# Kernel optimization log

Measured on AMD Instinct MI355X. Metric: run time of the kernel, lower is better.

The kernel has to match this reference:

```python
import jax, jax.numpy as jnp
import numpy as np

B, C, H, W = 8, 64, 128, 128
OUT, K, PAD = 128, 9, 1  # 3x3 kernel -> K=9 taps


def setup_inputs() -> dict:
    key = jax.random.key(0)
    ks = jax.random.split(key, 6)
    x = jax.random.normal(ks[0], (B, C, H, W), dtype=jnp.float32)
    # trained-like params: small random offsets (std ~1-2 px) and mask logits
    w_offset = jax.random.normal(ks[1], (2 * K, C, 3, 3), dtype=jnp.float32) * 0.05
    b_offset = jax.random.normal(ks[2], (2 * K,), dtype=jnp.float32) * 0.1
    w_mask = jax.random.normal(ks[3], (K, C, 3, 3), dtype=jnp.float32) * 0.05
    b_mask = jax.random.normal(ks[4], (K,), dtype=jnp.float32) * 0.1
    w_conv = jax.random.normal(ks[5], (OUT, C, 3, 3), dtype=jnp.float32) * (1.0 / np.sqrt(C * 9))
    return {"x": x, "w_offset": w_offset, "b_offset": b_offset,
            "w_mask": w_mask, "b_mask": b_mask, "w_conv": w_conv}


def _conv3x3(x, w, b):
    out = jax.lax.conv_general_dilated(
        x, w, window_strides=(1, 1), padding=((PAD, PAD), (PAD, PAD)),
        dimension_numbers=("NCHW", "OIHW", "NCHW"))
    return out + b[None, :, None, None]


def _bilinear_gather(img, gy, gx):
    # img: [C,H,W]; gy,gx: [K,H,W] float sampling coords (zero outside bounds)
    C_, H_, W_ = img.shape
    y0 = jnp.floor(gy)
    x0 = jnp.floor(gx)
    wy = gy - y0
    wx = gx - x0
    img_flat = img.reshape(C_, H_ * W_)

    def corner(yi, xi, wgt):
        valid = ((yi >= 0) & (yi < H_) & (xi >= 0) & (xi < W_)).astype(img.dtype)
        yc = jnp.clip(yi, 0, H_ - 1).astype(jnp.int32)
        xc = jnp.clip(xi, 0, W_ - 1).astype(jnp.int32)
        v = img_flat[:, yc * W_ + xc]  # [C,K,H,W]
        return v * (wgt * valid)[None]

    return (corner(y0, x0, (1 - wy) * (1 - wx))
            + corner(y0, x0 + 1, (1 - wy) * wx)
            + corner(y0 + 1, x0, wy * (1 - wx))
            + corner(y0 + 1, x0 + 1, wy * wx))  # [C,K,H,W]


def reference(x, w_offset, b_offset, w_mask, b_mask, w_conv):
    offset = _conv3x3(x, w_offset, b_offset)                  # [B,18,H,W]
    mask = jax.nn.sigmoid(_conv3x3(x, w_mask, b_mask))        # [B,9,H,W]
    B_, C_, H_, W_ = x.shape
    # torchvision layout: channel 2k = dy, 2k+1 = dx for kernel tap k
    off = offset.reshape(B_, K, 2, H_, W_)
    dy, dx = off[:, :, 0], off[:, :, 1]                       # [B,K,H,W]
    ky, kx = jnp.meshgrid(jnp.arange(3, dtype=x.dtype),
                          jnp.arange(3, dtype=x.dtype), indexing="ij")
    gy = jnp.arange(H_, dtype=x.dtype)[None, None, :, None] - PAD + ky.reshape(1, K, 1, 1) + dy
    gx = jnp.arange(W_, dtype=x.dtype)[None, None, None, :] - PAD + kx.reshape(1, K, 1, 1) + dx
    sampled = jax.vmap(_bilinear_gather)(x, gy, gx)           # [B,C,K,H,W]
    sampled = sampled * mask[:, None]                         # modulated (DCNv2)
    out = jnp.einsum("bckhw,ock->bohw", sampled, w_conv.reshape(OUT, C_, K))
    return out
```

## Files before the change

kernel.cpp:

```cpp
#include <hip/hip_runtime.h>
#include <math.h>

#define Himg 128
#define Wimg 128
#define HW   16384
#define Cin  64
#define Kk   9
#define OUTC 128
#define Bsz  8

typedef __attribute__((ext_vector_type(8))) _Float16 half8;
typedef __attribute__((ext_vector_type(4))) float   floatx4;

#define SPL8(v) ((half8){(v),(v),(v),(v),(v),(v),(v),(v)})

__global__ __launch_bounds__(256) void prep(const float* __restrict__ x,
                                            const float* __restrict__ w_conv,
                                            const float* __restrict__ w_offset,
                                            const float* __restrict__ w_mask,
                                            _Float16* __restrict__ xt,
                                            _Float16* __restrict__ wpk_h,
                                            _Float16* __restrict__ wpk2) {
    __shared__ _Float16 tile[Cin][130];
    int t   = threadIdx.x;
    int bid = blockIdx.x;

    if (bid < 1024) {
        int b = bid >> 7;
        int h = bid & 127;
        const float* xb = x + (size_t)b * Cin * HW + (size_t)h * Wimg;
#pragma unroll
        for (int j = 0; j < 32; ++j) {
            int e = t + j * 256;
            int c = e >> 7;
            int w = e & 127;
            tile[c][w] = (_Float16)xb[(size_t)c * HW + w];
        }
        __syncthreads();
        unsigned* dst = (unsigned*)xt + ((size_t)b * HW + (size_t)h * Wimg) * 32;
#pragma unroll
        for (int j = 0; j < 16; ++j) {
            int d  = t + j * 256;
            int w  = d >> 5;
            int cp = d & 31;
            union { unsigned u; _Float16 hh[2]; } pk;
            pk.hh[0] = tile[2 * cp][w];
            pk.hh[1] = tile[2 * cp + 1][w];
            dst[d] = pk.u;
        }
        return;
    }

    if (bid < 1024 + 288) {
        int idx = (bid - 1024) * 256 + t;
        if (idx < Kk * Cin * OUTC) {
            int i    = idx & 7;
            int l    = (idx >> 3) & 63;
            int g    = idx >> 9;
            int mt   = g & 7;
            int ch   = g >> 3;
            int kq   = l >> 4;
            int ln16 = l & 15;
            int o    = mt * 16 + ln16;
            int kl   = kq * 8 + i;
            int c    = (ch & 1) * 32 + kl;
            int kt   = ch >> 1;
            wpk_h[idx] = (_Float16)w_conv[(o * Cin + c) * 9 + kt];
        }
        return;
    }

    {
        int idx = (bid - 1312) * 256 + t;
        if (idx < 18 * 32 * 32) {
            int i    = idx & 7;
            int l    = (idx >> 3) & 63;
            int g    = idx >> 9;
            int mt0  = g & 1;
            int ch   = g >> 1;
            int kq   = l >> 4;
            int ln16 = l & 15;
            int m    = mt0 * 16 + ln16;
            int kl   = kq * 8 + i;
            int c    = (ch & 1) * 32 + kl;
            int kt   = ch >> 1;
            float v = 0.0f;
            if (m < 18)      v = w_offset[(m * Cin + c) * 9 + kt];
            else if (m < 27) v = w_mask[((m - 18) * Cin + c) * 9 + kt];
            wpk2[idx] = (_Float16)v;
        }
    }
}

__global__ __launch_bounds__(256, 3) void deform_fused(
        const _Float16* __restrict__ xt, const _Float16* __restrict__ wpk_h,
        const _Float16* __restrict__ wpk2,
        const float* __restrict__ b_offset, const float* __restrict__ b_mask,
        float* __restrict__ out) {
    __shared__ _Float16 Vw[4][2][16][40];
    __shared__ float    Pw[4][32][16];

    int t    = threadIdx.x;
    int bid  = blockIdx.x;
    int b    = bid & 7;
    int pb   = bid >> 3;
    int pix0 = pb * 64;
    int h    = pix0 >> 7;
    int w0   = pix0 & 127;

    int lane = t & 63;
    int wv   = t >> 6;
    int q    = t >> 2;
    int qloc = (lane >> 2) & 15;
    int c4   = t & 3;
    int kq   = lane >> 4;
    int ln16 = lane & 15;

    const _Float16* xtb  = xt + (size_t)b * HW * Cin;
    const half8* wsrc    = (const half8*)wpk_h;
    const half8* w2src   = (const half8*)wpk2;

    floatx4 acc2_0 = (floatx4){0.f, 0.f, 0.f, 0.f};
    floatx4 acc2_1 = (floatx4){0.f, 0.f, 0.f, 0.f};

    half8 pvA, pvB;

#define LOADX0(chn, DST) { \
    const int ktn = (chn) >> 1, cgn = (chn) & 1; \
    int row = h + (ktn / 3) - 1; \
    int col = w0 + q + (ktn % 3) - 1; \
    bool okc = (row >= 0) && (row < Himg) && (col >= 0) && (col < Wimg); \
    if (okc) DST = *(const half8*)(xtb + ((size_t)(row * Wimg + col)) * Cin \
                                   + cgn * 32 + c4 * 8); \
    else     DST = SPL8((_Float16)0.0f); \
}

#define P0STEP(ch, PV) { \
    half8 af0 = w2src[((size_t)(ch) * 2 + 0) * 64 + lane]; \
    half8 af1 = w2src[((size_t)(ch) * 2 + 1) * 64 + lane]; \
    *(half8*)&Vw[wv][(ch) & 1][qloc][c4 * 8] = PV; \
    if ((ch) < 16) LOADX0((ch) + 2, PV); \
    half8 bf = *(const half8*)&Vw[wv][(ch) & 1][ln16][kq * 8]; \
    acc2_0 = __builtin_amdgcn_mfma_f32_16x16x32_f16(af0, bf, acc2_0, 0, 0, 0); \
    acc2_1 = __builtin_amdgcn_mfma_f32_16x16x32_f16(af1, bf, acc2_1, 0, 0, 0); \
}

    LOADX0(0, pvA)
    LOADX0(1, pvB)

    P0STEP(0,  pvA) P0STEP(1,  pvB) P0STEP(2,  pvA) P0STEP(3,  pvB)
    P0STEP(4,  pvA) P0STEP(5,  pvB) P0STEP(6,  pvA) P0STEP(7,  pvB)
    P0STEP(8,  pvA) P0STEP(9,  pvB) P0STEP(10, pvA) P0STEP(11, pvB)
    P0STEP(12, pvA) P0STEP(13, pvB) P0STEP(14, pvA) P0STEP(15, pvB)
    P0STEP(16, pvA) P0STEP(17, pvB)

#pragma unroll
    for (int r = 0; r < 4; ++r) {
        Pw[wv][kq * 4 + r][ln16]      = acc2_0[r];
        Pw[wv][16 + kq * 4 + r][ln16] = acc2_1[r];
    }

    int      geomr[9];
    unsigned wab[9], wcd[9];
    {
        float fh = (float)h, fw = (float)(w0 + q);
#pragma unroll
        for (int k = 0; k < 9; ++k) {
            float dyv = Pw[wv][2 * k][qloc]     + b_offset[2 * k];
            float dxv = Pw[wv][2 * k + 1][qloc] + b_offset[2 * k + 1];
            float mz  = Pw[wv][18 + k][qloc]    + b_mask[k];
            float mkv = 1.0f / (1.0f + expf(-mz));

            float gy  = fh + (float)(k / 3) - 1.0f + dyv;
            float gx  = fw + (float)(k % 3) - 1.0f + dxv;
            float y0f = floorf(gy), x0f = floorf(gx);
            int   y0  = (int)y0f,   x0 = (int)x0f;
            float wy  = gy - y0f,   wx = gx - x0f;
            int   y1  = y0 + 1,     x1 = x0 + 1;

            bool vy0 = (y0 >= 0) && (y0 < Himg);
            bool vy1 = (y1 >= 0) && (y1 < Himg);
            bool vx0 = (x0 >= 0) && (x0 < Wimg);
            bool vx1 = (x1 >= 0) && (x1 < Wimg);

            float w00 = (vy0 && vx0) ? (1.0f - wy) * (1.0f - wx) * mkv : 0.0f;
            float w01 = (vy0 && vx1) ? (1.0f - wy) * wx          * mkv : 0.0f;
            float w10 = (vy1 && vx0) ? wy          * (1.0f - wx) * mkv : 0.0f;
            float w11 = (vy1 && vx1) ? wy          * wx          * mkv : 0.0f;

            int y0c = min(max(y0, 0), Himg - 1), y1c = min(max(y1, 0), Himg - 1);
            int x0c = min(max(x0, 0), Wimg - 1), x1c = min(max(x1, 0), Wimg - 1);
            geomr[k] = (y0c * Wimg + x0c) | ((x1c - x0c) << 14) | ((y1c - y0c) << 15);
            union { unsigned u; _Float16 hh[2]; } pk;
            pk.hh[0] = (_Float16)w00; pk.hh[1] = (_Float16)w01; wab[k] = pk.u;
            pk.hh[0] = (_Float16)w10; pk.hh[1] = (_Float16)w11; wcd[k] = pk.u;
        }
    }

    floatx4 acc[8];
#pragma unroll
    for (int i = 0; i < 8; ++i) acc[i] = (floatx4){0.f, 0.f, 0.f, 0.f};

    half8 gA0, gA1, gA2, gA3, gB0, gB1, gB2, gB3;

#define LOADG(chn, D0, D1, D2, D3) { \
    int gg = geomr[(chn) >> 1]; \
    const _Float16* xc = xtb + (size_t)(gg & 0x3fff) * Cin \
                         + ((chn) & 1) * 32 + c4 * 8; \
    int ob = (gg & 0x4000) >> 8;    \
    int oc = (gg & 0x8000) >> 2;    \
    D0 = *(const half8*)(xc); \
    D1 = *(const half8*)(xc + ob); \
    D2 = *(const half8*)(xc + oc); \
    D3 = *(const half8*)(xc + oc + ob); \
}

#define P1STEP(ch, G0, G1, G2, G3) { \
     \
    half8 ar0 = wsrc[((size_t)(ch) * 8 + 0) * 64 + lane]; \
    half8 ar1 = wsrc[((size_t)(ch) * 8 + 1) * 64 + lane]; \
    half8 ar2 = wsrc[((size_t)(ch) * 8 + 2) * 64 + lane]; \
    half8 ar3 = wsrc[((size_t)(ch) * 8 + 3) * 64 + lane]; \
    half8 ar4 = wsrc[((size_t)(ch) * 8 + 4) * 64 + lane]; \
    half8 ar5 = wsrc[((size_t)(ch) * 8 + 5) * 64 + lane]; \
    half8 ar6 = wsrc[((size_t)(ch) * 8 + 6) * 64 + lane]; \
    half8 ar7 = wsrc[((size_t)(ch) * 8 + 7) * 64 + lane]; \
    union { unsigned u; _Float16 hh[2]; } u1, u2; \
    u1.u = wab[(ch) >> 1];  u2.u = wcd[(ch) >> 1]; \
    half8 vv = G0 * SPL8(u1.hh[0]) + G1 * SPL8(u1.hh[1]) \
             + G2 * SPL8(u2.hh[0]) + G3 * SPL8(u2.hh[1]); \
    *(half8*)&Vw[wv][(ch) & 1][qloc][c4 * 8] = vv; \
    if ((ch) < 16) LOADG((ch) + 2, G0, G1, G2, G3); \
    half8 bf = *(const half8*)&Vw[wv][(ch) & 1][ln16][kq * 8]; \
    acc[0] = __builtin_amdgcn_mfma_f32_16x16x32_f16(ar0, bf, acc[0], 0, 0, 0); \
    acc[1] = __builtin_amdgcn_mfma_f32_16x16x32_f16(ar1, bf, acc[1], 0, 0, 0); \
    acc[2] = __builtin_amdgcn_mfma_f32_16x16x32_f16(ar2, bf, acc[2], 0, 0, 0); \
    acc[3] = __builtin_amdgcn_mfma_f32_16x16x32_f16(ar3, bf, acc[3], 0, 0, 0); \
    acc[4] = __builtin_amdgcn_mfma_f32_16x16x32_f16(ar4, bf, acc[4], 0, 0, 0); \
    acc[5] = __builtin_amdgcn_mfma_f32_16x16x32_f16(ar5, bf, acc[5], 0, 0, 0); \
    acc[6] = __builtin_amdgcn_mfma_f32_16x16x32_f16(ar6, bf, acc[6], 0, 0, 0); \
    acc[7] = __builtin_amdgcn_mfma_f32_16x16x32_f16(ar7, bf, acc[7], 0, 0, 0); \
}

    LOADG(0, gA0, gA1, gA2, gA3)
    LOADG(1, gB0, gB1, gB2, gB3)

    P1STEP(0,  gA0, gA1, gA2, gA3) P1STEP(1,  gB0, gB1, gB2, gB3)
    P1STEP(2,  gA0, gA1, gA2, gA3) P1STEP(3,  gB0, gB1, gB2, gB3)
    P1STEP(4,  gA0, gA1, gA2, gA3) P1STEP(5,  gB0, gB1, gB2, gB3)
    P1STEP(6,  gA0, gA1, gA2, gA3) P1STEP(7,  gB0, gB1, gB2, gB3)
    P1STEP(8,  gA0, gA1, gA2, gA3) P1STEP(9,  gB0, gB1, gB2, gB3)
    P1STEP(10, gA0, gA1, gA2, gA3) P1STEP(11, gB0, gB1, gB2, gB3)
    P1STEP(12, gA0, gA1, gA2, gA3) P1STEP(13, gB0, gB1, gB2, gB3)
    P1STEP(14, gA0, gA1, gA2, gA3) P1STEP(15, gB0, gB1, gB2, gB3)
    P1STEP(16, gA0, gA1, gA2, gA3) P1STEP(17, gB0, gB1, gB2, gB3)

#pragma unroll
    for (int mt = 0; mt < 8; ++mt) {
#pragma unroll
        for (int r = 0; r < 4; ++r) {
            int o = mt * 16 + kq * 4 + r;
            out[(size_t)(b * OUTC + o) * HW + pix0 + wv * 16 + ln16] = acc[mt][r];
        }
    }
}

extern "C" void kernel_launch(void* const* d_in, const int* in_sizes, int n_in,
                              void* d_out, int out_size, void* d_ws, size_t ws_size,
                              hipStream_t stream) {
    const float* x        = (const float*)d_in[0];
    const float* w_offset = (const float*)d_in[1];
    const float* b_offset = (const float*)d_in[2];
    const float* w_mask   = (const float*)d_in[3];
    const float* b_mask   = (const float*)d_in[4];
    const float* w_conv   = (const float*)d_in[5];
    float* out = (float*)d_out;

    _Float16* wpk_h = (_Float16*)d_ws;
    _Float16* wpk2  = wpk_h + 73728;
    _Float16* xtb   = wpk2 + 18432;

    prep<<<1384, 256, 0, stream>>>(x, w_conv, w_offset, w_mask, xtb, wpk_h, wpk2);
    deform_fused<<<2048, 256, 0, stream>>>(xtb, wpk_h, wpk2, b_offset, b_mask, out);
}
```

Baseline: 165.2 us.

## Stage main-GEMM weights through double-buffered LDS and prefetch offset-conv weights

```diff
diff --git a/kernel.cpp b/kernel.cpp
--- a/kernel.cpp
+++ b/kernel.cpp
@@ -98,7 +98,10 @@
         const float* __restrict__ b_offset, const float* __restrict__ b_mask,
         float* __restrict__ out) {
     __shared__ _Float16 Vw[4][2][16][40];
-    __shared__ float    Pw[4][32][16];
+    __shared__ union {
+        float    P[4][32][16];
+        _Float16 Wl[2][4096];
+    } sm2;
 
     int t    = threadIdx.x;
     int bid  = blockIdx.x;
@@ -123,7 +126,7 @@
     floatx4 acc2_0 = (floatx4){0.f, 0.f, 0.f, 0.f};
     floatx4 acc2_1 = (floatx4){0.f, 0.f, 0.f, 0.f};
 
-    half8 pvA, pvB;
+    half8 pvA, pvB, af0p, af1p;
 
 #define LOADX0(chn, DST) { \
     const int ktn = (chn) >> 1, cgn = (chn) & 1; \
@@ -136,17 +139,22 @@
 }
 
 #define P0STEP(ch, PV) { \
-    half8 af0 = w2src[((size_t)(ch) * 2 + 0) * 64 + lane]; \
-    half8 af1 = w2src[((size_t)(ch) * 2 + 1) * 64 + lane]; \
+    half8 af0c = af0p, af1c = af1p; \
     *(half8*)&Vw[wv][(ch) & 1][qloc][c4 * 8] = PV; \
     if ((ch) < 16) LOADX0((ch) + 2, PV); \
+    if ((ch) < 17) { \
+        af0p = w2src[((size_t)((ch) + 1) * 2 + 0) * 64 + lane]; \
+        af1p = w2src[((size_t)((ch) + 1) * 2 + 1) * 64 + lane]; \
+    } \
     half8 bf = *(const half8*)&Vw[wv][(ch) & 1][ln16][kq * 8]; \
-    acc2_0 = __builtin_amdgcn_mfma_f32_16x16x32_f16(af0, bf, acc2_0, 0, 0, 0); \
-    acc2_1 = __builtin_amdgcn_mfma_f32_16x16x32_f16(af1, bf, acc2_1, 0, 0, 0); \
+    acc2_0 = __builtin_amdgcn_mfma_f32_16x16x32_f16(af0c, bf, acc2_0, 0, 0, 0); \
+    acc2_1 = __builtin_amdgcn_mfma_f32_16x16x32_f16(af1c, bf, acc2_1, 0, 0, 0); \
 }
 
     LOADX0(0, pvA)
     LOADX0(1, pvB)
+    af0p = w2src[(size_t)0 * 64 + lane];
+    af1p = w2src[(size_t)1 * 64 + lane];
 
     P0STEP(0,  pvA) P0STEP(1,  pvB) P0STEP(2,  pvA) P0STEP(3,  pvB)
     P0STEP(4,  pvA) P0STEP(5,  pvB) P0STEP(6,  pvA) P0STEP(7,  pvB)
@@ -156,8 +164,8 @@
 
 #pragma unroll
     for (int r = 0; r < 4; ++r) {
-        Pw[wv][kq * 4 + r][ln16]      = acc2_0[r];
-        Pw[wv][16 + kq * 4 + r][ln16] = acc2_1[r];
+        sm2.P[wv][kq * 4 + r][ln16]      = acc2_0[r];
+        sm2.P[wv][16 + kq * 4 + r][ln16] = acc2_1[r];
     }
 
     int      geomr[9];
@@ -166,9 +174,9 @@
         float fh = (float)h, fw = (float)(w0 + q);
 #pragma unroll
         for (int k = 0; k < 9; ++k) {
-            float dyv = Pw[wv][2 * k][qloc]     + b_offset[2 * k];
-            float dxv = Pw[wv][2 * k + 1][qloc] + b_offset[2 * k + 1];
-            float mz  = Pw[wv][18 + k][qloc]    + b_mask[k];
+            float dyv = sm2.P[wv][2 * k][qloc]     + b_offset[2 * k];
+            float dxv = sm2.P[wv][2 * k + 1][qloc] + b_offset[2 * k + 1];
+            float mz  = sm2.P[wv][18 + k][qloc]    + b_mask[k];
             float mkv = 1.0f / (1.0f + expf(-mz));
 
             float gy  = fh + (float)(k / 3) - 1.0f + dyv;
@@ -201,7 +209,7 @@
 #pragma unroll
     for (int i = 0; i < 8; ++i) acc[i] = (floatx4){0.f, 0.f, 0.f, 0.f};
 
-    half8 gA0, gA1, gA2, gA3, gB0, gB1, gB2, gB3;
+    half8 gA0, gA1, gA2, gA3, gB0, gB1, gB2, gB3, wrA, wrB;
 
 #define LOADG(chn, D0, D1, D2, D3) { \
     int gg = geomr[(chn) >> 1]; \
@@ -215,35 +223,56 @@
     D3 = *(const half8*)(xc + oc + ob); \
 }
 
+#define LOADW(chn) { \
+    wrA = wsrc[(size_t)(chn) * 512 + t]; \
+    wrB = wsrc[(size_t)(chn) * 512 + 256 + t]; \
+}
+#define PUTW(bufi) { \
+    *(half8*)&sm2.Wl[bufi][t * 8]        = wrA; \
+    *(half8*)&sm2.Wl[bufi][2048 + t * 8] = wrB; \
+}
+
 #define P1STEP(ch, G0, G1, G2, G3) { \
      \
-    half8 ar0 = wsrc[((size_t)(ch) * 8 + 0) * 64 + lane]; \
-    half8 ar1 = wsrc[((size_t)(ch) * 8 + 1) * 64 + lane]; \
-    half8 ar2 = wsrc[((size_t)(ch) * 8 + 2) * 64 + lane]; \
-    half8 ar3 = wsrc[((size_t)(ch) * 8 + 3) * 64 + lane]; \
-    half8 ar4 = wsrc[((size_t)(ch) * 8 + 4) * 64 + lane]; \
-    half8 ar5 = wsrc[((size_t)(ch) * 8 + 5) * 64 + lane]; \
-    half8 ar6 = wsrc[((size_t)(ch) * 8 + 6) * 64 + lane]; \
-    half8 ar7 = wsrc[((size_t)(ch) * 8 + 7) * 64 + lane]; \
+    if ((ch) < 17) PUTW(((ch) + 1) & 1); \
+     \
     union { unsigned u; _Float16 hh[2]; } u1, u2; \
     u1.u = wab[(ch) >> 1];  u2.u = wcd[(ch) >> 1]; \
     half8 vv = G0 * SPL8(u1.hh[0]) + G1 * SPL8(u1.hh[1]) \
              + G2 * SPL8(u2.hh[0]) + G3 * SPL8(u2.hh[1]); \
     *(half8*)&Vw[wv][(ch) & 1][qloc][c4 * 8] = vv; \
+     \
     if ((ch) < 16) LOADG((ch) + 2, G0, G1, G2, G3); \
+    if ((ch) < 16) LOADW((ch) + 2); \
+     \
     half8 bf = *(const half8*)&Vw[wv][(ch) & 1][ln16][kq * 8]; \
-    acc[0] = __builtin_amdgcn_mfma_f32_16x16x32_f16(ar0, bf, acc[0], 0, 0, 0); \
-    acc[1] = __builtin_amdgcn_mfma_f32_16x16x32_f16(ar1, bf, acc[1], 0, 0, 0); \
-    acc[2] = __builtin_amdgcn_mfma_f32_16x16x32_f16(ar2, bf, acc[2], 0, 0, 0); \
-    acc[3] = __builtin_amdgcn_mfma_f32_16x16x32_f16(ar3, bf, acc[3], 0, 0, 0); \
-    acc[4] = __builtin_amdgcn_mfma_f32_16x16x32_f16(ar4, bf, acc[4], 0, 0, 0); \
-    acc[5] = __builtin_amdgcn_mfma_f32_16x16x32_f16(ar5, bf, acc[5], 0, 0, 0); \
-    acc[6] = __builtin_amdgcn_mfma_f32_16x16x32_f16(ar6, bf, acc[6], 0, 0, 0); \
-    acc[7] = __builtin_amdgcn_mfma_f32_16x16x32_f16(ar7, bf, acc[7], 0, 0, 0); \
-}
-
+    half8 a0 = *(const half8*)&sm2.Wl[(ch) & 1][0 * 512 + lane * 8]; \
+    half8 a1 = *(const half8*)&sm2.Wl[(ch) & 1][1 * 512 + lane * 8]; \
+    half8 a2 = *(const half8*)&sm2.Wl[(ch) & 1][2 * 512 + lane * 8]; \
+    half8 a3 = *(const half8*)&sm2.Wl[(ch) & 1][3 * 512 + lane * 8]; \
+    half8 a4 = *(const half8*)&sm2.Wl[(ch) & 1][4 * 512 + lane * 8]; \
+    half8 a5 = *(const half8*)&sm2.Wl[(ch) & 1][5 * 512 + lane * 8]; \
+    half8 a6 = *(const half8*)&sm2.Wl[(ch) & 1][6 * 512 + lane * 8]; \
+    half8 a7 = *(const half8*)&sm2.Wl[(ch) & 1][7 * 512 + lane * 8]; \
+    acc[0] = __builtin_amdgcn_mfma_f32_16x16x32_f16(a0, bf, acc[0], 0, 0, 0); \
+    acc[1] = __builtin_amdgcn_mfma_f32_16x16x32_f16(a1, bf, acc[1], 0, 0, 0); \
+    acc[2] = __builtin_amdgcn_mfma_f32_16x16x32_f16(a2, bf, acc[2], 0, 0, 0); \
+    acc[3] = __builtin_amdgcn_mfma_f32_16x16x32_f16(a3, bf, acc[3], 0, 0, 0); \
+    acc[4] = __builtin_amdgcn_mfma_f32_16x16x32_f16(a4, bf, acc[4], 0, 0, 0); \
+    acc[5] = __builtin_amdgcn_mfma_f32_16x16x32_f16(a5, bf, acc[5], 0, 0, 0); \
+    acc[6] = __builtin_amdgcn_mfma_f32_16x16x32_f16(a6, bf, acc[6], 0, 0, 0); \
+    acc[7] = __builtin_amdgcn_mfma_f32_16x16x32_f16(a7, bf, acc[7], 0, 0, 0); \
+    __syncthreads();    \
+}
+
+    __syncthreads();
+
+    LOADW(0)
+    PUTW(0)
+    LOADW(1)
     LOADG(0, gA0, gA1, gA2, gA3)
     LOADG(1, gB0, gB1, gB2, gB3)
+    __syncthreads();
 
     P1STEP(0,  gA0, gA1, gA2, gA3) P1STEP(1,  gB0, gB1, gB2, gB3)
     P1STEP(2,  gA0, gA1, gA2, gA3) P1STEP(3,  gB0, gB1, gB2, gB3)
```

New measurement: 201.5 us. 22.0% more time.

## Double per-wave pixel tile to 32 to reuse weight fragments across two MFMA groups

Applied to the files above, without the earlier changes.

```diff
diff --git a/kernel.cpp b/kernel.cpp
--- a/kernel.cpp
+++ b/kernel.cpp
@@ -11,6 +11,7 @@
 
 typedef __attribute__((ext_vector_type(8))) _Float16 half8;
 typedef __attribute__((ext_vector_type(4))) float   floatx4;
+typedef __attribute__((ext_vector_type(4))) int     intx4;
 
 #define SPL8(v) ((half8){(v),(v),(v),(v),(v),(v),(v),(v)})
 
@@ -92,83 +93,99 @@
     }
 }
 
-__global__ __launch_bounds__(256, 3) void deform_fused(
+__global__ __launch_bounds__(256, 2) void deform_fused(
         const _Float16* __restrict__ xt, const _Float16* __restrict__ wpk_h,
         const _Float16* __restrict__ wpk2,
         const float* __restrict__ b_offset, const float* __restrict__ b_mask,
         float* __restrict__ out) {
-    __shared__ _Float16 Vw[4][2][16][40];
-    __shared__ float    Pw[4][32][16];
+    __shared__ _Float16 Vw[4][2][32][40];
+    __shared__ float    Pw[4][32][32];
+    __shared__ int      Geo[4][9][32][4];
 
     int t    = threadIdx.x;
     int bid  = blockIdx.x;
     int b    = bid & 7;
     int pb   = bid >> 3;
-    int pix0 = pb * 64;
-    int h    = pix0 >> 7;
-    int w0   = pix0 & 127;
+    int pix0 = pb << 7;
+    int h    = pb;
 
     int lane = t & 63;
     int wv   = t >> 6;
-    int q    = t >> 2;
-    int qloc = (lane >> 2) & 15;
-    int c4   = t & 3;
+    int qloc = lane >> 2;
+    int c4   = lane & 3;
     int kq   = lane >> 4;
     int ln16 = lane & 15;
+    int sp0  = wv * 32;
 
     const _Float16* xtb  = xt + (size_t)b * HW * Cin;
     const half8* wsrc    = (const half8*)wpk_h;
     const half8* w2src   = (const half8*)wpk2;
 
-    floatx4 acc2_0 = (floatx4){0.f, 0.f, 0.f, 0.f};
-    floatx4 acc2_1 = (floatx4){0.f, 0.f, 0.f, 0.f};
-
-    half8 pvA, pvB;
-
-#define LOADX0(chn, DST) { \
+    floatx4 acc2_00 = (floatx4){0.f,0.f,0.f,0.f};
+    floatx4 acc2_10 = (floatx4){0.f,0.f,0.f,0.f};
+    floatx4 acc2_01 = (floatx4){0.f,0.f,0.f,0.f};
+    floatx4 acc2_11 = (floatx4){0.f,0.f,0.f,0.f};
+
+    half8 pvA0, pvB0, pvA1, pvB1, af0p, af1p;
+
+#define LOADX0(chn, g, DST) { \
     const int ktn = (chn) >> 1, cgn = (chn) & 1; \
     int row = h + (ktn / 3) - 1; \
-    int col = w0 + q + (ktn % 3) - 1; \
+    int col = sp0 + (g) * 16 + qloc + (ktn % 3) - 1; \
     bool okc = (row >= 0) && (row < Himg) && (col >= 0) && (col < Wimg); \
     if (okc) DST = *(const half8*)(xtb + ((size_t)(row * Wimg + col)) * Cin \
                                    + cgn * 32 + c4 * 8); \
     else     DST = SPL8((_Float16)0.0f); \
 }
 
-#define P0STEP(ch, PV) { \
-    half8 af0 = w2src[((size_t)(ch) * 2 + 0) * 64 + lane]; \
-    half8 af1 = w2src[((size_t)(ch) * 2 + 1) * 64 + lane]; \
-    *(half8*)&Vw[wv][(ch) & 1][qloc][c4 * 8] = PV; \
-    if ((ch) < 16) LOADX0((ch) + 2, PV); \
-    half8 bf = *(const half8*)&Vw[wv][(ch) & 1][ln16][kq * 8]; \
-    acc2_0 = __builtin_amdgcn_mfma_f32_16x16x32_f16(af0, bf, acc2_0, 0, 0, 0); \
-    acc2_1 = __builtin_amdgcn_mfma_f32_16x16x32_f16(af1, bf, acc2_1, 0, 0, 0); \
-}
-
-    LOADX0(0, pvA)
-    LOADX0(1, pvB)
-
-    P0STEP(0,  pvA) P0STEP(1,  pvB) P0STEP(2,  pvA) P0STEP(3,  pvB)
-    P0STEP(4,  pvA) P0STEP(5,  pvB) P0STEP(6,  pvA) P0STEP(7,  pvB)
-    P0STEP(8,  pvA) P0STEP(9,  pvB) P0STEP(10, pvA) P0STEP(11, pvB)
-    P0STEP(12, pvA) P0STEP(13, pvB) P0STEP(14, pvA) P0STEP(15, pvB)
-    P0STEP(16, pvA) P0STEP(17, pvB)
+#define P0STEP(ch, PV0, PV1) { \
+    half8 af0c = af0p, af1c = af1p; \
+    *(half8*)&Vw[wv][(ch) & 1][qloc][c4 * 8]      = PV0; \
+    *(half8*)&Vw[wv][(ch) & 1][16 + qloc][c4 * 8] = PV1; \
+    if ((ch) < 16) { LOADX0((ch) + 2, 0, PV0) LOADX0((ch) + 2, 1, PV1) } \
+    if ((ch) < 17) { \
+        af0p = w2src[((size_t)((ch) + 1) * 2 + 0) * 64 + lane]; \
+        af1p = w2src[((size_t)((ch) + 1) * 2 + 1) * 64 + lane]; \
+    } \
+    half8 bf0 = *(const half8*)&Vw[wv][(ch) & 1][ln16][kq * 8]; \
+    half8 bf1 = *(const half8*)&Vw[wv][(ch) & 1][16 + ln16][kq * 8]; \
+    acc2_00 = __builtin_amdgcn_mfma_f32_16x16x32_f16(af0c, bf0, acc2_00, 0, 0, 0); \
+    acc2_10 = __builtin_amdgcn_mfma_f32_16x16x32_f16(af1c, bf0, acc2_10, 0, 0, 0); \
+    acc2_01 = __builtin_amdgcn_mfma_f32_16x16x32_f16(af0c, bf1, acc2_01, 0, 0, 0); \
+    acc2_11 = __builtin_amdgcn_mfma_f32_16x16x32_f16(af1c, bf1, acc2_11, 0, 0, 0); \
+}
+
+    LOADX0(0, 0, pvA0) LOADX0(0, 1, pvA1)
+    LOADX0(1, 0, pvB0) LOADX0(1, 1, pvB1)
+    af0p = w2src[(size_t)0 * 64 + lane];
+    af1p = w2src[(size_t)1 * 64 + lane];
+
+    P0STEP(0,  pvA0, pvA1) P0STEP(1,  pvB0, pvB1)
+    P0STEP(2,  pvA0, pvA1) P0STEP(3,  pvB0, pvB1)
+    P0STEP(4,  pvA0, pvA1) P0STEP(5,  pvB0, pvB1)
+    P0STEP(6,  pvA0, pvA1) P0STEP(7,  pvB0, pvB1)
+    P0STEP(8,  pvA0, pvA1) P0STEP(9,  pvB0, pvB1)
+    P0STEP(10, pvA0, pvA1) P0STEP(11, pvB0, pvB1)
+    P0STEP(12, pvA0, pvA1) P0STEP(13, pvB0, pvB1)
+    P0STEP(14, pvA0, pvA1) P0STEP(15, pvB0, pvB1)
+    P0STEP(16, pvA0, pvA1) P0STEP(17, pvB0, pvB1)
 
 #pragma unroll
     for (int r = 0; r < 4; ++r) {
-        Pw[wv][kq * 4 + r][ln16]      = acc2_0[r];
-        Pw[wv][16 + kq * 4 + r][ln16] = acc2_1[r];
-    }
-
-    int      geomr[9];
-    unsigned wab[9], wcd[9];
+        Pw[wv][kq * 4 + r][ln16]           = acc2_00[r];
+        Pw[wv][16 + kq * 4 + r][ln16]      = acc2_10[r];
+        Pw[wv][kq * 4 + r][16 + ln16]      = acc2_01[r];
+        Pw[wv][16 + kq * 4 + r][16 + ln16] = acc2_11[r];
+    }
+
     {
-        float fh = (float)h, fw = (float)(w0 + q);
+        int pxg = lane >> 1;
+        float fh = (float)h, fw = (float)(sp0 + pxg);
 #pragma unroll
         for (int k = 0; k < 9; ++k) {
-            float dyv = Pw[wv][2 * k][qloc]     + b_offset[2 * k];
-            float dxv = Pw[wv][2 * k + 1][qloc] + b_offset[2 * k + 1];
-            float mz  = Pw[wv][18 + k][qloc]    + b_mask[k];
+            float dyv = Pw[wv][2 * k][pxg]     + b_offset[2 * k];
+            float dxv = Pw[wv][2 * k + 1][pxg] + b_offset[2 * k + 1];
+            float mz  = Pw[wv][18 + k][pxg]    + b_mask[k];
             float mkv = 1.0f / (1.0f + expf(-mz));
 
             float gy  = fh + (float)(k / 3) - 1.0f + dyv;
@@ -190,21 +207,33 @@
 
             int y0c = min(max(y0, 0), Himg - 1), y1c = min(max(y1, 0), Himg - 1);
             int x0c = min(max(x0, 0), Wimg - 1), x1c = min(max(x1, 0), Wimg - 1);
-            geomr[k] = (y0c * Wimg + x0c) | ((x1c - x0c) << 14) | ((y1c - y0c) << 15);
+            int geom = (y0c * Wimg + x0c) | ((x1c - x0c) << 14) | ((y1c - y0c) << 15);
             union { unsigned u; _Float16 hh[2]; } pk;
-            pk.hh[0] = (_Float16)w00; pk.hh[1] = (_Float16)w01; wab[k] = pk.u;
-            pk.hh[0] = (_Float16)w10; pk.hh[1] = (_Float16)w11; wcd[k] = pk.u;
-        }
-    }
-
-    floatx4 acc[8];
-#pragma unroll
-    for (int i = 0; i < 8; ++i) acc[i] = (floatx4){0.f, 0.f, 0.f, 0.f};
-
-    half8 gA0, gA1, gA2, gA3, gB0, gB1, gB2, gB3;
-
-#define LOADG(chn, D0, D1, D2, D3) { \
-    int gg = geomr[(chn) >> 1]; \
+            int wabk, wcdk;
+            pk.hh[0] = (_Float16)w00; pk.hh[1] = (_Float16)w01; wabk = (int)pk.u;
+            pk.hh[0] = (_Float16)w10; pk.hh[1] = (_Float16)w11; wcdk = (int)pk.u;
+            if ((lane & 1) == 0) {
+                Geo[wv][k][pxg][0] = geom;
+                Geo[wv][k][pxg][1] = wabk;
+                Geo[wv][k][pxg][2] = wcdk;
+            }
+        }
+    }
+
+    floatx4 acc[8][2];
+#pragma unroll
+    for (int i = 0; i < 8; ++i) {
+        acc[i][0] = (floatx4){0.f,0.f,0.f,0.f};
+        acc[i][1] = (floatx4){0.f,0.f,0.f,0.f};
+    }
+
+    half8 gA0, gA1, gA2, gA3;
+    half8 gB0, gB1, gB2, gB3;
+    half8 gC0, gC1, gC2, gC3;
+    half8 gD0, gD1, gD2, gD3;
+
+#define LOADG(chn, g, D0, D1, D2, D3) { \
+    int gg = Geo[wv][(chn) >> 1][(g) * 16 + qloc][0]; \
     const _Float16* xc = xtb + (size_t)(gg & 0x3fff) * Cin \
                          + ((chn) & 1) * 32 + c4 * 8; \
     int ob = (gg & 0x4000) >> 8;    \
@@ -215,52 +244,87 @@
     D3 = *(const half8*)(xc + oc + ob); \
 }
 
-#define P1STEP(ch, G0, G1, G2, G3) { \
+#define P1STEP(ch, A0, A1, A2, A3, C0, C1, C2, C3) { \
      \
-    half8 ar0 = wsrc[((size_t)(ch) * 8 + 0) * 64 + lane]; \
-    half8 ar1 = wsrc[((size_t)(ch) * 8 + 1) * 64 + lane]; \
-    half8 ar2 = wsrc[((size_t)(ch) * 8 + 2) * 64 + lane]; \
-    half8 ar3 = wsrc[((size_t)(ch) * 8 + 3) * 64 + lane]; \
-    half8 ar4 = wsrc[((size_t)(ch) * 8 + 4) * 64 + lane]; \
-    half8 ar5 = wsrc[((size_t)(ch) * 8 + 5) * 64 + lane]; \
-    half8 ar6 = wsrc[((size_t)(ch) * 8 + 6) * 64 + lane]; \
-    half8 ar7 = wsrc[((size_t)(ch) * 8 + 7) * 64 + lane]; \
+    half8 w_0 = wsrc[((size_t)(ch) * 8 + 0) * 64 + lane]; \
+    half8 w_1 = wsrc[((size_t)(ch) * 8 + 1) * 64 + lane]; \
+    half8 w_2 = wsrc[((size_t)(ch) * 8 + 2) * 64 + lane]; \
+    half8 w_3 = wsrc[((size_t)(ch) * 8 + 3) * 64 + lane]; \
+    half8 w_4 = wsrc[((size_t)(ch) * 8 + 4) * 64 + lane]; \
+    half8 w_5 = wsrc[((size_t)(ch) * 8 + 5) * 64 + lane]; \
+    half8 w_6 = wsrc[((size_t)(ch) * 8 + 6) * 64 + lane]; \
+    half8 w_7 = wsrc[((size_t)(ch) * 8 + 7) * 64 + lane]; \
+     \
+    intx4 q0 = *(const intx4*)&Geo[wv][(ch) >> 1][qloc][0]; \
+    intx4 q1 = *(const intx4*)&Geo[wv][(ch) >> 1][16 + qloc][0]; \
     union { unsigned u; _Float16 hh[2]; } u1, u2; \
-    u1.u = wab[(ch) >> 1];  u2.u = wcd[(ch) >> 1]; \
-    half8 vv = G0 * SPL8(u1.hh[0]) + G1 * SPL8(u1.hh[1]) \
-             + G2 * SPL8(u2.hh[0]) + G3 * SPL8(u2.hh[1]); \
-    *(half8*)&Vw[wv][(ch) & 1][qloc][c4 * 8] = vv; \
-    if ((ch) < 16) LOADG((ch) + 2, G0, G1, G2, G3); \
-    half8 bf = *(const half8*)&Vw[wv][(ch) & 1][ln16][kq * 8]; \
-    acc[0] = __builtin_amdgcn_mfma_f32_16x16x32_f16(ar0, bf, acc[0], 0, 0, 0); \
-    acc[1] = __builtin_amdgcn_mfma_f32_16x16x32_f16(ar1, bf, acc[1], 0, 0, 0); \
-    acc[2] = __builtin_amdgcn_mfma_f32_16x16x32_f16(ar2, bf, acc[2], 0, 0, 0); \
-    acc[3] = __builtin_amdgcn_mfma_f32_16x16x32_f16(ar3, bf, acc[3], 0, 0, 0); \
-    acc[4] = __builtin_amdgcn_mfma_f32_16x16x32_f16(ar4, bf, acc[4], 0, 0, 0); \
-    acc[5] = __builtin_amdgcn_mfma_f32_16x16x32_f16(ar5, bf, acc[5], 0, 0, 0); \
-    acc[6] = __builtin_amdgcn_mfma_f32_16x16x32_f16(ar6, bf, acc[6], 0, 0, 0); \
-    acc[7] = __builtin_amdgcn_mfma_f32_16x16x32_f16(ar7, bf, acc[7], 0, 0, 0); \
-}
-
-    LOADG(0, gA0, gA1, gA2, gA3)
-    LOADG(1, gB0, gB1, gB2, gB3)
-
-    P1STEP(0,  gA0, gA1, gA2, gA3) P1STEP(1,  gB0, gB1, gB2, gB3)
-    P1STEP(2,  gA0, gA1, gA2, gA3) P1STEP(3,  gB0, gB1, gB2, gB3)
-    P1STEP(4,  gA0, gA1, gA2, gA3) P1STEP(5,  gB0, gB1, gB2, gB3)
-    P1STEP(6,  gA0, gA1, gA2, gA3) P1STEP(7,  gB0, gB1, gB2, gB3)
-    P1STEP(8,  gA0, gA1, gA2, gA3) P1STEP(9,  gB0, gB1, gB2, gB3)
-    P1STEP(10, gA0, gA1, gA2, gA3) P1STEP(11, gB0, gB1, gB2, gB3)
-    P1STEP(12, gA0, gA1, gA2, gA3) P1STEP(13, gB0, gB1, gB2, gB3)
-    P1STEP(14, gA0, gA1, gA2, gA3) P1STEP(15, gB0, gB1, gB2, gB3)
-    P1STEP(16, gA0, gA1, gA2, gA3) P1STEP(17, gB0, gB1, gB2, gB3)
+    u1.u = (unsigned)q0.y;  u2.u = (unsigned)q0.z; \
+    half8 vv0 = A0 * SPL8(u1.hh[0]) + A1 * SPL8(u1.hh[1]) \
+              + A2 * SPL8(u2.hh[0]) + A3 * SPL8(u2.hh[1]); \
+    *(half8*)&Vw[wv][(ch) & 1][qloc][c4 * 8] = vv0; \
+    u1.u = (unsigned)q1.y;  u2.u = (unsigned)q1.z; \
+    half8 vv1 = C0 * SPL8(u1.hh[0]) + C1 * SPL8(u1.hh[1]) \
+              + C2 * SPL8(u2.hh[0]) + C3 * SPL8(u2.hh[1]); \
+    *(half8*)&Vw[wv][(ch) & 1][16 + qloc][c4 * 8] = vv1; \
+     \
+    if ((ch) < 16) { \
+        LOADG((ch) + 2, 0, A0, A1, A2, A3) \
+        LOADG((ch) + 2, 1, C0, C1, C2, C3) \
+    } \
+    half8 bf0 = *(const half8*)&Vw[wv][(ch) & 1][ln16][kq * 8]; \
+    half8 bf1 = *(const half8*)&Vw[wv][(ch) & 1][16 + ln16][kq * 8]; \
+    acc[0][0] = __builtin_amdgcn_mfma_f32_16x16x32_f16(w_0, bf0, acc[0][0], 0, 0, 0); \
+    acc[1][0] = __builtin_amdgcn_mfma_f32_16x16x32_f16(w_1, bf0, acc[1][0], 0, 0, 0); \
+    acc[2][0] = __builtin_amdgcn_mfma_f32_16x16x32_f16(w_2, bf0, acc[2][0], 0, 0, 0); \
+    acc[3][0] = __builtin_amdgcn_mfma_f32_16x16x32_f16(w_3, bf0, acc[3][0], 0, 0, 0); \
+    acc[4][0] = __builtin_amdgcn_mfma_f32_16x16x32_f16(w_4, bf0, acc[4][0], 0, 0, 0); \
+    acc[5][0] = __builtin_amdgcn_mfma_f32_16x16x32_f16(w_5, bf0, acc[5][0], 0, 0, 0); \
+    acc[6][0] = __builtin_amdgcn_mfma_f32_16x16x32_f16(w_6, bf0, acc[6][0], 0, 0, 0); \
+    acc[7][0] = __builtin_amdgcn_mfma_f32_16x16x32_f16(w_7, bf0, acc[7][0], 0, 0, 0); \
+    acc[0][1] = __builtin_amdgcn_mfma_f32_16x16x32_f16(w_0, bf1, acc[0][1], 0, 0, 0); \
+    acc[1][1] = __builtin_amdgcn_mfma_f32_16x16x32_f16(w_1, bf1, acc[1][1], 0, 0, 0); \
+    acc[2][1] = __builtin_amdgcn_mfma_f32_16x16x32_f16(w_2, bf1, acc[2][1], 0, 0, 0); \
+    acc[3][1] = __builtin_amdgcn_mfma_f32_16x16x32_f16(w_3, bf1, acc[3][1], 0, 0, 0); \
+    acc[4][1] = __builtin_amdgcn_mfma_f32_16x16x32_f16(w_4, bf1, acc[4][1], 0, 0, 0); \
+    acc[5][1] = __builtin_amdgcn_mfma_f32_16x16x32_f16(w_5, bf1, acc[5][1], 0, 0, 0); \
+    acc[6][1] = __builtin_amdgcn_mfma_f32_16x16x32_f16(w_6, bf1, acc[6][1], 0, 0, 0); \
+    acc[7][1] = __builtin_amdgcn_mfma_f32_16x16x32_f16(w_7, bf1, acc[7][1], 0, 0, 0); \
+}
+
+    LOADG(0, 0, gA0, gA1, gA2, gA3)
+    LOADG(0, 1, gC0, gC1, gC2, gC3)
+    LOADG(1, 0, gB0, gB1, gB2, gB3)
+    LOADG(1, 1, gD0, gD1, gD2, gD3)
+
+    P1STEP(0,  gA0, gA1, gA2, gA3, gC0, gC1, gC2, gC3)
+    P1STEP(1,  gB0, gB1, gB2, gB3, gD0, gD1, gD2, gD3)
+    P1STEP(2,  gA0, gA1, gA2, gA3, gC0, gC1, gC2, gC3)
+    P1STEP(3,  gB0, gB1, gB2, gB3, gD0, gD1, gD2, gD3)
+    P1STEP(4,  gA0, gA1, gA2, gA3, gC0, gC1, gC2, gC3)
+    P1STEP(5,  gB0, gB1, gB2, gB3, gD0, gD1, gD2, gD3)
+    P1STEP(6,  gA0, gA1, gA2, gA3, gC0, gC1, gC2, gC3)
+    P1STEP(7,  gB0, gB1, gB2, gB3, gD0, gD1, gD2, gD3)
+    P1STEP(8,  gA0, gA1, gA2, gA3, gC0, gC1, gC2, gC3)
+    P1STEP(9,  gB0, gB1, gB2, gB3, gD0, gD1, gD2, gD3)
+    P1STEP(10, gA0, gA1, gA2, gA3, gC0, gC1, gC2, gC3)
+    P1STEP(11, gB0, gB1, gB2, gB3, gD0, gD1, gD2, gD3)
+    P1STEP(12, gA0, gA1, gA2, gA3, gC0, gC1, gC2, gC3)
+    P1STEP(13, gB0, gB1, gB2, gB3, gD0, gD1, gD2, gD3)
+    P1STEP(14, gA0, gA1, gA2, gA3, gC0, gC1, gC2, gC3)
+    P1STEP(15, gB0, gB1, gB2, gB3, gD0, gD1, gD2, gD3)
+    P1STEP(16, gA0, gA1, gA2, gA3, gC0, gC1, gC2, gC3)
+    P1STEP(17, gB0, gB1, gB2, gB3, gD0, gD1, gD2, gD3)
 
 #pragma unroll
     for (int mt = 0; mt < 8; ++mt) {
 #pragma unroll
-        for (int r = 0; r < 4; ++r) {
-            int o = mt * 16 + kq * 4 + r;
-            out[(size_t)(b * OUTC + o) * HW + pix0 + wv * 16 + ln16] = acc[mt][r];
+        for (int g = 0; g < 2; ++g) {
+#pragma unroll
+            for (int r = 0; r < 4; ++r) {
+                int o = mt * 16 + kq * 4 + r;
+                out[(size_t)(b * OUTC + o) * HW + pix0 + sp0 + g * 16 + ln16]
+                    = acc[mt][g][r];
+            }
         }
     }
 }
@@ -281,5 +345,5 @@
     _Float16* xtb   = wpk2 + 18432;
 
     prep<<<1384, 256, 0, stream>>>(x, w_conv, w_offset, w_mask, xtb, wpk_h, wpk2);
-    deform_fused<<<2048, 256, 0, stream>>>(xtb, wpk_h, wpk2, b_offset, b_mask, out);
-}
+    deform_fused<<<1024, 256, 0, stream>>>(xtb, wpk_h, wpk2, b_offset, b_mask, out);
+}
```

After: 156.8 us. 1.05x faster.
